# Optimization experiments

Measured on AMD Instinct MI355X. Metric: run time of the kernel, lower is better.

The kernel has to match this reference:

```python
import jax, jax.numpy as jnp
import numpy as np

N_NODES = 50000
N_EDGES = 800000
D = 64               # in_channels
CHEB_ORDER = 16
NUM_GRAPHS = 100
SCALES = [2, 4, 8, 16]           # 2**i for i in 1..4
FENG = np.array([4, 8, 9, 12, 13, 14])  # feng_filters()


def _cheb_coeffs(order):
    # FastScatterW1._get_coeffs with N = cheb_order + 1
    N = order + 1
    a1, a2 = 1.0, 1.0        # a_arange = [0, 2]
    tmp = np.arange(N)
    num = np.cos(np.pi * (tmp + 0.5) / N)
    xs = a1 * num + a2
    c = np.zeros((len(SCALES), N))
    for si, s in enumerate(SCALES):
        ker = np.sqrt(np.clip((1.0 - xs) ** (s // 2) - (1.0 - xs) ** s, 0.0, None))
        for o in range(N):
            c[si, o] = 2.0 / N * np.dot(ker, np.cos(np.pi * o * (tmp + 0.5) / N))
    return c.T.astype(np.float32)  # [order+1, n_scales]


def setup_inputs():
    key = jax.random.key(0)
    k1, k2 = jax.random.split(key)
    x = jax.random.normal(k1, (N_NODES, D), dtype=jnp.float32)
    edge_index = jax.random.randint(k2, (2, N_EDGES), 0, N_NODES, dtype=jnp.int32)
    # 100 contiguous graphs of 500 nodes each (sorted, every graph non-empty)
    batch = (jnp.arange(N_NODES) // (N_NODES // NUM_GRAPHS)).astype(jnp.int32)
    return {"x": x, "edge_index": edge_index, "batch": batch}


def _cheb_apply(x, rows, cols, w, coeffs, n):
    # ChebConvFixed recurrence with arange=[0,1] -> a1 = a2 = 0.5.
    # x: [N, F] -> out: [S, N, F]
    def prop(h):  # scatter-add message passing: out[c] += w_e * h[row_e]
        return jax.ops.segment_sum(w[:, None] * h[rows], cols, num_segments=n)
    Tx0 = x
    Tx1 = 2.0 * prop(x) - x                      # (prop(x) - a2*Tx0)/a1
    out = coeffs[0][:, None, None] * (0.5 * Tx0) + coeffs[1][:, None, None] * Tx1
    def step(carry, c_k):
        t0, t1, acc = carry
        t2 = 4.0 * (prop(t1) - 0.5 * t1) - t0    # 2/a1 * (prop - a2*t1) - t0
        return (t1, t2, acc + c_k[:, None, None] * t2), None
    (_, _, out), _ = jax.lax.scan(step, (Tx0, Tx1, out), coeffs[2:])
    return out


def _scatter_moments(f, batch, g):
    # f: [N, F] node features, vectorized version of scatter_moments(..., 4)
    cnt = jax.ops.segment_sum(jnp.ones((f.shape[0],), f.dtype), batch, num_segments=g)[:, None]
    mean = jax.ops.segment_sum(f, batch, num_segments=g) / cnt
    dev = f - mean[batch]
    m2 = jax.ops.segment_sum(dev ** 2, batch, num_segments=g) / cnt
    m3 = jax.ops.segment_sum(dev ** 3, batch, num_segments=g) / cnt
    m4 = jax.ops.segment_sum(dev ** 4, batch, num_segments=g) / cnt
    safe = jnp.where(m2 > 0, m2, 1.0)
    skew = jnp.where(m2 > 0, m3 / safe ** 1.5, 0.0)
    skew = jnp.where(skew > 1e15, 0.0, skew)
    kurt = jnp.where(m2 > 0, m4 / safe ** 2 - 3.0, -3.0)
    kurt = jnp.where(kurt > 1e15, -3.0, kurt)
    return jnp.concatenate([mean, m2, skew, kurt], axis=1)  # [G, 4F]


def reference(x, edge_index, batch):
    n = x.shape[0]
    row, col = edge_index[0], edge_index[1]
    # symmetric normalization: deg from scatter_add of unit weights on col
    deg = jax.ops.segment_sum(jnp.ones((row.shape[0],), x.dtype), col, num_segments=n)
    dh = jnp.where(deg > 0, deg ** -0.5, 0.0)
    ew = dh[row] * dh[col]
    # Original: add_self_loops(+1), /2, then negate and add_self_loops(+1) again:
    # edge weights -> -ew/2 on real edges; net self-loop weight = -0.5 + 1.0 = 0.5.
    loops = jnp.arange(n, dtype=row.dtype)
    rows_all = jnp.concatenate([row, loops])
    cols_all = jnp.concatenate([col, loops])
    w = jnp.concatenate([-0.5 * ew, 0.5 * jnp.ones((n,), x.dtype)])
    coeffs = jnp.asarray(_cheb_coeffs(CHEB_ORDER))  # [K+1, 4]
    # alpha = 0 -> deg0 = deg1 = deg**0 = 1, so pre/post degree scalings are identity.
    d1 = _cheb_apply(x, rows_all, cols_all, w, coeffs, n)              # [4, N, D]
    s1 = jnp.abs(d1)
    h = s1.transpose(1, 0, 2).reshape(n, 4 * D)                         # [N, 4D]
    d2 = _cheb_apply(h, rows_all, cols_all, w, coeffs, n)               # [4, N, 4D]
    s2 = jnp.abs(d2).transpose(1, 0, 2).reshape(n, 16, D)[:, jnp.asarray(FENG)]  # [N, 6, D]
    feat = jnp.concatenate([x[:, None, :], s1.transpose(1, 0, 2), s2], axis=1)  # [N, 11, D]
    return _scatter_moments(feat.reshape(n, -1), batch, NUM_GRAPHS)    # [G, 44*D]
```

## Files before the change

### kernel.cpp

```cpp
#include <hip/hip_runtime.h>
#include <math.h>

#define NN 50000
#define NE 800000
#define NGRAPH 100
#define NPG 500
#define NB_SCAN 196
#define NCHUNK 5
#define NPC 100
#define CHAIN_ELEMS ((size_t)NN * 64)
#define CH4 ((size_t)NN * 16)
#define GRID_PROP (NN / 4)
#define GRID_P163 (NN / 8)

typedef long long ll;
typedef _Float16 h4_t __attribute__((ext_vector_type(4)));
typedef _Float16 h8_t __attribute__((ext_vector_type(8)));

__device__ __forceinline__ void unpack(ll v, int& r, float& w) {
    r = (int)(v & 0xffffffffLL);
    w = __int_as_float((int)(v >> 32));
}

__device__ __forceinline__ float4 f4fma(float w, float4 v, float4 a) {
    a.x += w * v.x; a.y += w * v.y; a.z += w * v.z; a.w += w * v.w;
    return a;
}

__device__ __forceinline__ float4 h4f4(h4_t h) {
    return make_float4((float)h.x, (float)h.y, (float)h.z, (float)h.w);
}

__device__ __forceinline__ h4_t f4h4(float4 v) {
    h4_t h;
    h.x = (_Float16)v.x; h.y = (_Float16)v.y;
    h.z = (_Float16)v.z; h.w = (_Float16)v.w;
    return h;
}


__global__ void k_deg(const int* __restrict__ col, int* __restrict__ degi) {
    int e = blockIdx.x * blockDim.x + threadIdx.x;
    if (e < NE) atomicAdd(&degi[col[e]], 1);
}

__global__ void k_dh(const int* __restrict__ degi, float* __restrict__ dh) {
    int i = blockIdx.x * blockDim.x + threadIdx.x;
    if (i < NN) {
        int d = degi[i];
        dh[i] = d > 0 ? (float)(1.0 / sqrt((double)d)) : 0.0f;
    }
}

__global__ void k_bsum(const int* __restrict__ cnt, int* __restrict__ bsum) {
    __shared__ int sh[256];
    int i = blockIdx.x * 256 + threadIdx.x;
    sh[threadIdx.x] = (i < NN) ? cnt[i] : 0;
    __syncthreads();
    for (int s = 128; s > 0; s >>= 1) {
        if (threadIdx.x < s) sh[threadIdx.x] += sh[threadIdx.x + s];
        __syncthreads();
    }
    if (threadIdx.x == 0) bsum[blockIdx.x] = sh[0];
}

__global__ void k_bscan(const int* __restrict__ bsum, int* __restrict__ boff) {
    __shared__ int sh[2][256];
    int v = (threadIdx.x < NB_SCAN) ? bsum[threadIdx.x] : 0;
    int cur = 0;
    sh[0][threadIdx.x] = v;
    __syncthreads();
    for (int s = 1; s < 256; s <<= 1) {
        int val = sh[cur][threadIdx.x];
        if ((int)threadIdx.x >= s) val += sh[cur][threadIdx.x - s];
        sh[cur ^ 1][threadIdx.x] = val;
        cur ^= 1;
        __syncthreads();
    }
    if (threadIdx.x < NB_SCAN) boff[threadIdx.x] = sh[cur][threadIdx.x] - v;
}

__global__ void k_scan2(const int* __restrict__ cnt, const int* __restrict__ boff,
                        int* __restrict__ off) {
    __shared__ int sh[2][256];
    int i = blockIdx.x * 256 + threadIdx.x;
    int v = (i < NN) ? cnt[i] : 0;
    int cur = 0;
    sh[0][threadIdx.x] = v;
    __syncthreads();
    for (int s = 1; s < 256; s <<= 1) {
        int val = sh[cur][threadIdx.x];
        if ((int)threadIdx.x >= s) val += sh[cur][threadIdx.x - s];
        sh[cur ^ 1][threadIdx.x] = val;
        cur ^= 1;
        __syncthreads();
    }
    if (i < NN) off[i] = boff[blockIdx.x] + sh[cur][threadIdx.x] - v;
}

__global__ void k_fill(const int* __restrict__ row, const int* __restrict__ col,
                       const float* __restrict__ dh, const int* __restrict__ off,
                       int* __restrict__ cursor, ll* __restrict__ csrp) {
    int e = blockIdx.x * blockDim.x + threadIdx.x;
    if (e >= NE) return;
    int r = row[e], c = col[e];
    int pos = off[c] + atomicAdd(&cursor[c], 1);
    float w = dh[r] * dh[c];
    csrp[pos] = ((ll)__float_as_int(w) << 32) | (unsigned int)r;
}


template <bool INIT>
__global__ __launch_bounds__(256) void k_prop(
    const float* __restrict__ Tcur, const float* __restrict__ Tprev,
    float* __restrict__ Tnext, const int* __restrict__ off,
    const int* __restrict__ degi, const ll* __restrict__ csrp) {
    int node = blockIdx.x * 4 + (threadIdx.x >> 6);
    int lane = threadIdx.x & 63;
    int eg = lane >> 4;
    int cq = lane & 15;
    int s = off[node], e = s + degi[node];
    const float* tb = Tcur + (size_t)cq * 4;
    float4 a0 = make_float4(0.f, 0.f, 0.f, 0.f);
    float4 a1 = make_float4(0.f, 0.f, 0.f, 0.f);
    float4 pv = INIT ? make_float4(0.f, 0.f, 0.f, 0.f)
                     : *(const float4*)&Tprev[(size_t)node * 64 + cq * 4];
    int i = s;
    for (; i + 8 <= e; i += 8) {
        int r0, r1; float w0, w1;
        unpack(csrp[i + eg], r0, w0);
        unpack(csrp[i + 4 + eg], r1, w1);
        float4 v0 = *(const float4*)(tb + (size_t)r0 * 64);
        float4 v1 = *(const float4*)(tb + (size_t)r1 * 64);
        a0 = f4fma(w0, v0, a0);
        a1 = f4fma(w1, v1, a1);
    }
    for (; i < e; i += 4) {
        int idx = i + eg;
        bool act = idx < e;
        int r; float w;
        unpack(csrp[act ? idx : (e - 1)], r, w);
        if (!act) w = 0.f;
        float4 v = *(const float4*)(tb + (size_t)r * 64);
        a0 = f4fma(w, v, a0);
    }
    float4 g = make_float4(a0.x + a1.x, a0.y + a1.y, a0.z + a1.z, a0.w + a1.w);
    g.x += __shfl_xor(g.x, 16); g.y += __shfl_xor(g.y, 16);
    g.z += __shfl_xor(g.z, 16); g.w += __shfl_xor(g.w, 16);
    g.x += __shfl_xor(g.x, 32); g.y += __shfl_xor(g.y, 32);
    g.z += __shfl_xor(g.z, 32); g.w += __shfl_xor(g.w, 32);
    float4 t;
    if (INIT) {
        t = make_float4(-g.x, -g.y, -g.z, -g.w);
    } else {
        t = make_float4(-2.f * g.x - pv.x, -2.f * g.y - pv.y,
                        -2.f * g.z - pv.z, -2.f * g.w - pv.w);
    }
    if (eg == 0) *(float4*)&Tnext[(size_t)node * 64 + cq * 4] = t;
}


template <bool INIT>
__global__ __launch_bounds__(256) void k_prop16x3(
    const _Float16* __restrict__ Tcur, const _Float16* __restrict__ Tprev,
    _Float16* __restrict__ Tnext, const int* __restrict__ off,
    const int* __restrict__ degi, const ll* __restrict__ csrp) {
    int wav = blockIdx.x * 4 + (threadIdx.x >> 6);
    int lane = threadIdx.x & 63;
    int ns = lane >> 5;
    int eg = (lane >> 3) & 3;
    int cq = lane & 7;
    int node = wav * 2 + ns;
    int s = off[node], e = s + degi[node];
    const _Float16* tb0 = Tcur + (size_t)cq * 8;
    const _Float16* tb1 = tb0 + CHAIN_ELEMS;
    const _Float16* tb2 = tb0 + 2 * CHAIN_ELEMS;
    float aA[3][8], aB[3][8];
#pragma unroll
    for (int p = 0; p < 3; ++p)
#pragma unroll
        for (int j = 0; j < 8; ++j) { aA[p][j] = 0.f; aB[p][j] = 0.f; }
    int i = s;
    for (; i + 8 <= e; i += 8) {
        int r0, r1; float w0, w1;
        unpack(csrp[i + eg], r0, w0);
        unpack(csrp[i + 4 + eg], r1, w1);
        size_t o0 = (size_t)r0 * 64, o1 = (size_t)r1 * 64;
        h8_t h00 = *(const h8_t*)(tb0 + o0);
        h8_t h01 = *(const h8_t*)(tb1 + o0);
        h8_t h02 = *(const h8_t*)(tb2 + o0);
        h8_t h10 = *(const h8_t*)(tb0 + o1);
        h8_t h11 = *(const h8_t*)(tb1 + o1);
        h8_t h12 = *(const h8_t*)(tb2 + o1);
#pragma unroll
        for (int j = 0; j < 8; ++j) aA[0][j] += w0 * (float)h00[j];
#pragma unroll
        for (int j = 0; j < 8; ++j) aA[1][j] += w0 * (float)h01[j];
#pragma unroll
        for (int j = 0; j < 8; ++j) aA[2][j] += w0 * (float)h02[j];
#pragma unroll
        for (int j = 0; j < 8; ++j) aB[0][j] += w1 * (float)h10[j];
#pragma unroll
        for (int j = 0; j < 8; ++j) aB[1][j] += w1 * (float)h11[j];
#pragma unroll
        for (int j = 0; j < 8; ++j) aB[2][j] += w1 * (float)h12[j];
    }
    for (; i < e; i += 4) {
        int idx = i + eg;
        bool act = idx < e;
        int r; float w;
        unpack(csrp[act ? idx : (e - 1)], r, w);
        if (!act) w = 0.f;
        size_t o = (size_t)r * 64;
        h8_t h0 = *(const h8_t*)(tb0 + o);
        h8_t h1 = *(const h8_t*)(tb1 + o);
        h8_t h2 = *(const h8_t*)(tb2 + o);
#pragma unroll
        for (int j = 0; j < 8; ++j) aA[0][j] += w * (float)h0[j];
#pragma unroll
        for (int j = 0; j < 8; ++j) aA[1][j] += w * (float)h1[j];
#pragma unroll
        for (int j = 0; j < 8; ++j) aA[2][j] += w * (float)h2[j];
    }
    float g[3][8];
#pragma unroll
    for (int p = 0; p < 3; ++p)
#pragma unroll
        for (int j = 0; j < 8; ++j) g[p][j] = aA[p][j] + aB[p][j];
#pragma unroll
    for (int p = 0; p < 3; ++p)
#pragma unroll
        for (int j = 0; j < 8; ++j) {
            g[p][j] += __shfl_xor(g[p][j], 8);
            g[p][j] += __shfl_xor(g[p][j], 16);
        }
    if ((lane & 24) == 0) {
        size_t ob = (size_t)node * 64 + (size_t)cq * 8;
#pragma unroll
        for (int p = 0; p < 3; ++p) {
            size_t o = ob + (size_t)p * CHAIN_ELEMS;
            h8_t t;
            if (INIT) {
#pragma unroll
                for (int j = 0; j < 8; ++j) t[j] = (_Float16)(-g[p][j]);
            } else {
                h8_t ph = *(const h8_t*)&Tprev[o];
#pragma unroll
                for (int j = 0; j < 8; ++j)
                    t[j] = (_Float16)(-2.f * g[p][j] - (float)ph[j]);
            }
            *(h8_t*)&Tnext[o] = t;
        }
    }
}


struct CombCfg {
    float c0[4];
    float ck[4][8];
    int   plane[4];
};

template <int NS, int NT>
__global__ __launch_bounds__(256) void k_combine(
    const float4* __restrict__ src0, const float4* __restrict__ pool,
    float4* __restrict__ accb, _Float16* __restrict__ h16out,
    CombCfg cfg, int first, int doabs) {
    size_t v = (size_t)blockIdx.x * 256 + threadIdx.x;
    float4 tv[NS];
#pragma unroll
    for (int m = 0; m < NS; ++m) tv[m] = pool[(size_t)m * CH4 + v];
    float4 s0 = first ? src0[v] : make_float4(0.f, 0.f, 0.f, 0.f);
#pragma unroll
    for (int t = 0; t < NT; ++t) {
        size_t o = (size_t)cfg.plane[t] * CH4 + v;
        float4 a;
        if (first) {
            float c = cfg.c0[t];
            a = make_float4(c * s0.x, c * s0.y, c * s0.z, c * s0.w);
        } else {
            a = accb[o];
        }
#pragma unroll
        for (int m = 0; m < NS; ++m) a = f4fma(cfg.ck[t][m], tv[m], a);
        if (doabs) a = make_float4(fabsf(a.x), fabsf(a.y), fabsf(a.z), fabsf(a.w));
        accb[o] = a;
        if (doabs && h16out && cfg.plane[t] < 3) {
            size_t eo = (size_t)cfg.plane[t] * CHAIN_ELEMS + v * 4;
            *(h4_t*)&h16out[eo] = f4h4(a);
        }
    }
}


struct Comb316Cfg {
    float c0[6];
    float ck[6][4];
};

__global__ __launch_bounds__(256) void k_comb316(
    const float4* __restrict__ src0, const h4_t* __restrict__ pool,
    h4_t* __restrict__ accb, Comb316Cfg cfg, int first, int doabs) {
    size_t v = (size_t)blockIdx.x * 256 + threadIdx.x;
    float4 tv[4][3];
#pragma unroll
    for (int m = 0; m < 4; ++m)
#pragma unroll
        for (int sp = 0; sp < 3; ++sp)
            tv[m][sp] = h4f4(pool[((size_t)m * 3 + sp) * CH4 + v]);
    float4 s0[3];
    if (first) {
#pragma unroll
        for (int sp = 0; sp < 3; ++sp) s0[sp] = src0[(size_t)sp * CH4 + v];
    }
    const int SP[6] = {0, 0, 0, 1, 1, 2};
    const int PL[6] = {0, 1, 3, 2, 4, 5};
#pragma unroll
    for (int t = 0; t < 6; ++t) {
        size_t o = (size_t)PL[t] * CH4 + v;
        float4 a;
        if (first) {
            float c = cfg.c0[t];
            float4 s = s0[SP[t]];
            a = make_float4(c * s.x, c * s.y, c * s.z, c * s.w);
        } else {
            a = h4f4(accb[o]);
        }
#pragma unroll
        for (int m = 0; m < 4; ++m) a = f4fma(cfg.ck[t][m], tv[m][SP[t]], a);
        if (doabs) a = make_float4(fabsf(a.x), fabsf(a.y), fabsf(a.z), fabsf(a.w));
        accb[o] = f4h4(a);
    }
}


__global__ void k_mompart(const float* __restrict__ x, const float* __restrict__ hacc,
                          const _Float16* __restrict__ acc2, double* __restrict__ pmom) {
    int g = blockIdx.y;
    int c = blockIdx.z;
    int col = blockIdx.x * 256 + threadIdx.x;
    if (col >= 704) return;
    int base = g * NPG + c * NPC;
    double s1 = 0, s2 = 0, s3 = 0, s4 = 0;
    if (col < 320) {
        const float* src;
        int c0;
        if (col < 64) { src = x; c0 = col; }
        else { int p = (col - 64) >> 6; src = hacc + (size_t)p * CHAIN_ELEMS; c0 = (col - 64) & 63; }
        for (int i = 0; i < NPC; ++i) {
            double v = (double)src[(size_t)(base + i) * 64 + c0];
            double v2 = v * v;
            s1 += v; s2 += v2; s3 += v2 * v; s4 += v2 * v2;
        }
    } else {
        int p = (col - 320) >> 6;
        int c0 = (col - 320) & 63;
        const _Float16* src = acc2 + (size_t)p * CHAIN_ELEMS;
        for (int i = 0; i < NPC; ++i) {
            double v = (double)(float)src[(size_t)(base + i) * 64 + c0];
            double v2 = v * v;
            s1 += v; s2 += v2; s3 += v2 * v; s4 += v2 * v2;
        }
    }
    size_t ob = (((size_t)c * NGRAPH + g) * 704 + col) * 4;
    pmom[ob + 0] = s1;
    pmom[ob + 1] = s2;
    pmom[ob + 2] = s3;
    pmom[ob + 3] = s4;
}

__global__ void k_momfin(const double* __restrict__ pmom, float* __restrict__ out) {
    int g = blockIdx.y;
    int col = blockIdx.x * 256 + threadIdx.x;
    if (col >= 704) return;
    double s1 = 0, s2 = 0, s3 = 0, s4 = 0;
    for (int c = 0; c < NCHUNK; ++c) {
        size_t ob = (((size_t)c * NGRAPH + g) * 704 + col) * 4;
        s1 += pmom[ob + 0];
        s2 += pmom[ob + 1];
        s3 += pmom[ob + 2];
        s4 += pmom[ob + 3];
    }
    double n = (double)NPG;
    double mu = s1 / n;
    double E2 = s2 / n, E3 = s3 / n, E4 = s4 / n;
    double m2 = E2 - mu * mu;
    double m3 = E3 - 3.0 * mu * E2 + 2.0 * mu * mu * mu;
    double m4 = E4 - 4.0 * mu * E3 + 6.0 * mu * mu * E2 - 3.0 * mu * mu * mu * mu;
    float m2f = (float)m2;
    float skew = 0.f, kurt = -3.f;
    if (m2f > 0.f) {
        skew = (float)(m3 / (m2 * sqrt(m2)));
        if (skew > 1e15f) skew = 0.f;
        kurt = (float)(m4 / (m2 * m2) - 3.0);
        if (kurt > 1e15f) kurt = -3.f;
    }
    size_t ob = (size_t)g * 2816 + col;
    out[ob]        = (float)mu;
    out[ob + 704]  = m2f;
    out[ob + 1408] = skew;
    out[ob + 2112] = kurt;
}


extern "C" void kernel_launch(void* const* d_in, const int* in_sizes, int n_in,
                              void* d_out, int out_size, void* d_ws, size_t ws_size,
                              hipStream_t stream) {
    const float* x = (const float*)d_in[0];
    const int* ei  = (const int*)d_in[1];
    const int* row = ei;
    const int* col = ei + NE;
    float* out = (float*)d_out;

    float C[17][4];
    {
        const int Nc = 17;
        const int scales[4] = {2, 4, 8, 16};
        for (int si = 0; si < 4; ++si) {
            double ker[17];
            for (int j = 0; j < Nc; ++j) {
                double num = cos(M_PI * (j + 0.5) / Nc);
                double b = -num;
                double v = pow(b, (double)(scales[si] / 2)) - pow(b, (double)scales[si]);
                if (v < 0) v = 0;
                ker[j] = sqrt(v);
            }
            for (int o = 0; o < Nc; ++o) {
                double acc = 0;
                for (int j = 0; j < Nc; ++j) acc += ker[j] * cos(M_PI * o * (j + 0.5) / Nc);
                C[o][si] = (float)(2.0 / Nc * acc);
            }
        }
    }

    int*   degi; float* dh; int* off; int* cursor; int* bsum; int* boff;
    ll*    csrp; char* ub = nullptr;
    float* hacc; _Float16* acc2;
    int CAD1 = 8;
    const size_t H16B  = ((size_t)3 * CHAIN_ELEMS * 2 + 255) & ~(size_t)255;
    const size_t P16B  = ((size_t)12 * CHAIN_ELEMS * 2 + 255) & ~(size_t)255;
    const size_t PMOMB = (size_t)NCHUNK * NGRAPH * 704 * 4 * 8;
    size_t H16OFF = 0;
    for (int attempt = 0; attempt < 2; ++attempt) {
        CAD1 = (attempt == 0) ? 8 : 4;
        size_t POOLB = ((size_t)CAD1 * CHAIN_ELEMS * 4 + 255) & ~(size_t)255;
        H16OFF = (POOLB > P16B) ? POOLB : P16B;
        size_t UNB = H16OFF + H16B;
        if (PMOMB > UNB) UNB = PMOMB;
        char* p = (char*)d_ws;
        auto alloc = [&](size_t bytes) -> void* {
            void* r = (void*)p;
            p += (bytes + 255) & ~(size_t)255;
            return r;
        };
        degi   = (int*)alloc((size_t)NN * 4);
        dh     = (float*)alloc((size_t)NN * 4);
        off    = (int*)alloc((size_t)NN * 4);
        cursor = (int*)alloc((size_t)NN * 4);
        bsum   = (int*)alloc((size_t)NB_SCAN * 4);
        boff   = (int*)alloc((size_t)NB_SCAN * 4);
        csrp   = (ll*)alloc((size_t)NE * 8);
        ub     = (char*)alloc(UNB);
        hacc   = (float*)alloc((size_t)4 * CHAIN_ELEMS * 4);
        acc2   = (_Float16*)alloc((size_t)6 * CHAIN_ELEMS * 2);
        if ((size_t)(p - (char*)d_ws) <= ws_size) break;
    }
    float*    pool   = (float*)ub;
    _Float16* pool16 = (_Float16*)ub;
    _Float16* h16    = (_Float16*)(ub + H16OFF);
    double*   pmom   = (double*)ub;

    hipMemsetAsync(degi, 0, (size_t)NN * 4, stream);
    hipMemsetAsync(cursor, 0, (size_t)NN * 4, stream);

    k_deg  <<<(NE + 255) / 256, 256, 0, stream>>>(col, degi);
    k_dh   <<<(NN + 255) / 256, 256, 0, stream>>>(degi, dh);
    k_bsum <<<NB_SCAN, 256, 0, stream>>>(degi, bsum);
    k_bscan<<<1, 256, 0, stream>>>(bsum, boff);
    k_scan2<<<NB_SCAN, 256, 0, stream>>>(degi, boff, off);
    k_fill <<<(NE + 255) / 256, 256, 0, stream>>>(row, col, dh, off, cursor, csrp);

    const int GRID_C = (int)(CH4 / 256);

    auto slot = [&](int k) {
        return pool + (size_t)((k - 1) & (CAD1 - 1)) * CHAIN_ELEMS;
    };

    {
        const int scl[4] = {0, 1, 2, 3};
        k_prop<true><<<GRID_PROP, 256, 0, stream>>>(x, nullptr, slot(1),
                                                    off, degi, csrp);
        for (int k = 2; k <= 16; ++k) {
            const float* Tprev = (k == 2) ? x : slot(k - 2);
            k_prop<false><<<GRID_PROP, 256, 0, stream>>>(slot(k - 1), Tprev,
                                                         slot(k), off, degi, csrp);
            if ((k % CAD1) == 0) {
                CombCfg cfg;
                for (int t = 0; t < 4; ++t) {
                    int si = scl[t];
                    cfg.c0[t] = 0.5f * C[0][si];
                    cfg.plane[t] = t;
                    for (int m = 0; m < CAD1; ++m)
                        cfg.ck[t][m] = C[k - CAD1 + 1 + m][si];
                }
                int first = (k == CAD1) ? 1 : 0;
                int doabs = (k == 16) ? 1 : 0;
                _Float16* ho = doabs ? h16 : nullptr;
                if (CAD1 == 8)
                    k_combine<8, 4><<<GRID_C, 256, 0, stream>>>(
                        (const float4*)x, (const float4*)pool, (float4*)hacc,
                        ho, cfg, first, doabs);
                else
                    k_combine<4, 4><<<GRID_C, 256, 0, stream>>>(
                        (const float4*)x, (const float4*)pool, (float4*)hacc,
                        ho, cfg, first, doabs);
            }
        }
    }

    {
        auto slot3 = [&](int k) {
            return pool16 + (size_t)((k - 1) & 3) * 3 * CHAIN_ELEMS;
        };
        k_prop16x3<true><<<GRID_P163, 256, 0, stream>>>(h16, nullptr, slot3(1),
                                                        off, degi, csrp);
        for (int k = 2; k <= 16; ++k) {
            const _Float16* Tprev = (k == 2) ? h16 : slot3(k - 2);
            k_prop16x3<false><<<GRID_P163, 256, 0, stream>>>(slot3(k - 1), Tprev,
                                                             slot3(k), off, degi, csrp);
            if ((k % 4) == 0) {
                Comb316Cfg cfg;
                const int SI[6] = {1, 2, 3, 2, 3, 3};
                for (int t = 0; t < 6; ++t) {
                    cfg.c0[t] = 0.5f * C[0][SI[t]];
                    for (int m = 0; m < 4; ++m) cfg.ck[t][m] = C[k - 3 + m][SI[t]];
                }
                k_comb316<<<GRID_C, 256, 0, stream>>>(
                    (const float4*)hacc, (const h4_t*)pool16, (h4_t*)acc2,
                    cfg, (k == 4) ? 1 : 0, (k == 16) ? 1 : 0);
            }
        }
    }

    dim3 mg1(3, NGRAPH, NCHUNK);
    k_mompart<<<mg1, 256, 0, stream>>>(x, hacc, acc2, pmom);
    dim3 mg2(3, NGRAPH);
    k_momfin<<<mg2, 256, 0, stream>>>(pmom, out);
}
```

Measured before the change: 1.567 ms.

## Store first-stage Chebyshev chain in fp16 and remap prop to two nodes per wave

The first-layer Chebyshev recurrence now keeps x and every T_k in half precision, with fp32 accumulation. The propagation kernel is rewritten so each wave handles two nodes with 8-wide half vectors, and the combine kernel reads the fp16 pool. This halves the bytes per gathered neighbour row in the bandwidth-bound sparse propagation and shrinks the pool buffer, which removes the CAD1 fallback. The cost is fp16 rounding error compounding across the 16-step recurrence, plus an extra conversion pass over x.

Result: faster. 1.385 ms (-11.6%).

```diff
diff --git a/kernel.cpp b/kernel.cpp
--- a/kernel.cpp
+++ b/kernel.cpp
@@ -10,7 +10,6 @@
 #define NPC 100
 #define CHAIN_ELEMS ((size_t)NN * 64)
 #define CH4 ((size_t)NN * 16)
-#define GRID_PROP (NN / 4)
 #define GRID_P163 (NN / 8)
 
 typedef long long ll;
@@ -109,31 +108,40 @@
     csrp[pos] = ((ll)__float_as_int(w) << 32) | (unsigned int)r;
 }
 
+__global__ void k_tohalf(const float* __restrict__ src, _Float16* __restrict__ dst) {
+    size_t i = ((size_t)blockIdx.x * 256 + threadIdx.x) * 4;
+    float4 v = *(const float4*)&src[i];
+    *(h4_t*)&dst[i] = f4h4(v);
+}
+
 
 template <bool INIT>
-__global__ __launch_bounds__(256) void k_prop(
-    const float* __restrict__ Tcur, const float* __restrict__ Tprev,
-    float* __restrict__ Tnext, const int* __restrict__ off,
+__global__ __launch_bounds__(256) void k_prop16s(
+    const _Float16* __restrict__ Tcur, const _Float16* __restrict__ Tprev,
+    _Float16* __restrict__ Tnext, const int* __restrict__ off,
     const int* __restrict__ degi, const ll* __restrict__ csrp) {
-    int node = blockIdx.x * 4 + (threadIdx.x >> 6);
+    int wav = blockIdx.x * 4 + (threadIdx.x >> 6);
     int lane = threadIdx.x & 63;
-    int eg = lane >> 4;
-    int cq = lane & 15;
+    int ns = lane >> 5;
+    int eg = (lane >> 3) & 3;
+    int cq = lane & 7;
+    int node = wav * 2 + ns;
     int s = off[node], e = s + degi[node];
-    const float* tb = Tcur + (size_t)cq * 4;
-    float4 a0 = make_float4(0.f, 0.f, 0.f, 0.f);
-    float4 a1 = make_float4(0.f, 0.f, 0.f, 0.f);
-    float4 pv = INIT ? make_float4(0.f, 0.f, 0.f, 0.f)
-                     : *(const float4*)&Tprev[(size_t)node * 64 + cq * 4];
+    const _Float16* tb = Tcur + (size_t)cq * 8;
+    float accA[8], accB[8];
+#pragma unroll
+    for (int j = 0; j < 8; ++j) { accA[j] = 0.f; accB[j] = 0.f; }
     int i = s;
     for (; i + 8 <= e; i += 8) {
         int r0, r1; float w0, w1;
         unpack(csrp[i + eg], r0, w0);
         unpack(csrp[i + 4 + eg], r1, w1);
-        float4 v0 = *(const float4*)(tb + (size_t)r0 * 64);
-        float4 v1 = *(const float4*)(tb + (size_t)r1 * 64);
-        a0 = f4fma(w0, v0, a0);
-        a1 = f4fma(w1, v1, a1);
+        h8_t h0 = *(const h8_t*)(tb + (size_t)r0 * 64);
+        h8_t h1 = *(const h8_t*)(tb + (size_t)r1 * 64);
+#pragma unroll
+        for (int j = 0; j < 8; ++j) accA[j] += w0 * (float)h0[j];
+#pragma unroll
+        for (int j = 0; j < 8; ++j) accB[j] += w1 * (float)h1[j];
     }
     for (; i < e; i += 4) {
         int idx = i + eg;
@@ -141,22 +149,32 @@
         int r; float w;
         unpack(csrp[act ? idx : (e - 1)], r, w);
         if (!act) w = 0.f;
-        float4 v = *(const float4*)(tb + (size_t)r * 64);
-        a0 = f4fma(w, v, a0);
-    }
-    float4 g = make_float4(a0.x + a1.x, a0.y + a1.y, a0.z + a1.z, a0.w + a1.w);
-    g.x += __shfl_xor(g.x, 16); g.y += __shfl_xor(g.y, 16);
-    g.z += __shfl_xor(g.z, 16); g.w += __shfl_xor(g.w, 16);
-    g.x += __shfl_xor(g.x, 32); g.y += __shfl_xor(g.y, 32);
-    g.z += __shfl_xor(g.z, 32); g.w += __shfl_xor(g.w, 32);
-    float4 t;
-    if (INIT) {
-        t = make_float4(-g.x, -g.y, -g.z, -g.w);
-    } else {
-        t = make_float4(-2.f * g.x - pv.x, -2.f * g.y - pv.y,
-                        -2.f * g.z - pv.z, -2.f * g.w - pv.w);
-    }
-    if (eg == 0) *(float4*)&Tnext[(size_t)node * 64 + cq * 4] = t;
+        h8_t h = *(const h8_t*)(tb + (size_t)r * 64);
+#pragma unroll
+        for (int j = 0; j < 8; ++j) accA[j] += w * (float)h[j];
+    }
+    float g[8];
+#pragma unroll
+    for (int j = 0; j < 8; ++j) g[j] = accA[j] + accB[j];
+#pragma unroll
+    for (int j = 0; j < 8; ++j) {
+        g[j] += __shfl_xor(g[j], 8);
+        g[j] += __shfl_xor(g[j], 16);
+    }
+    if ((lane & 24) == 0) {
+        size_t o = (size_t)node * 64 + (size_t)cq * 8;
+        h8_t t;
+        if (INIT) {
+#pragma unroll
+            for (int j = 0; j < 8; ++j) t[j] = (_Float16)(-g[j]);
+        } else {
+            h8_t ph = *(const h8_t*)&Tprev[o];
+#pragma unroll
+            for (int j = 0; j < 8; ++j)
+                t[j] = (_Float16)(-2.f * g[j] - (float)ph[j]);
+        }
+        *(h8_t*)&Tnext[o] = t;
+    }
 }
 
 
@@ -262,14 +280,14 @@
 };
 
 template <int NS, int NT>
-__global__ __launch_bounds__(256) void k_combine(
-    const float4* __restrict__ src0, const float4* __restrict__ pool,
+__global__ __launch_bounds__(256) void k_combine16p1(
+    const float4* __restrict__ src0, const h4_t* __restrict__ pool,
     float4* __restrict__ accb, _Float16* __restrict__ h16out,
     CombCfg cfg, int first, int doabs) {
     size_t v = (size_t)blockIdx.x * 256 + threadIdx.x;
     float4 tv[NS];
 #pragma unroll
-    for (int m = 0; m < NS; ++m) tv[m] = pool[(size_t)m * CH4 + v];
+    for (int m = 0; m < NS; ++m) tv[m] = h4f4(pool[(size_t)m * CH4 + v]);
     float4 s0 = first ? src0[v] : make_float4(0.f, 0.f, 0.f, 0.f);
 #pragma unroll
     for (int t = 0; t < NT; ++t) {
@@ -435,16 +453,13 @@
 
     int*   degi; float* dh; int* off; int* cursor; int* bsum; int* boff;
     ll*    csrp; char* ub = nullptr;
-    float* hacc; _Float16* acc2;
-    int CAD1 = 8;
+    _Float16* x16; float* hacc; _Float16* acc2;
     const size_t H16B  = ((size_t)3 * CHAIN_ELEMS * 2 + 255) & ~(size_t)255;
+    const size_t P1B   = ((size_t)8 * CHAIN_ELEMS * 2 + 255) & ~(size_t)255;
     const size_t P16B  = ((size_t)12 * CHAIN_ELEMS * 2 + 255) & ~(size_t)255;
     const size_t PMOMB = (size_t)NCHUNK * NGRAPH * 704 * 4 * 8;
-    size_t H16OFF = 0;
-    for (int attempt = 0; attempt < 2; ++attempt) {
-        CAD1 = (attempt == 0) ? 8 : 4;
-        size_t POOLB = ((size_t)CAD1 * CHAIN_ELEMS * 4 + 255) & ~(size_t)255;
-        H16OFF = (POOLB > P16B) ? POOLB : P16B;
+    size_t H16OFF = (P1B > P16B) ? P1B : P16B;
+    {
         size_t UNB = H16OFF + H16B;
         if (PMOMB > UNB) UNB = PMOMB;
         char* p = (char*)d_ws;
@@ -461,11 +476,11 @@
         boff   = (int*)alloc((size_t)NB_SCAN * 4);
         csrp   = (ll*)alloc((size_t)NE * 8);
         ub     = (char*)alloc(UNB);
+        x16    = (_Float16*)alloc(CHAIN_ELEMS * 2);
         hacc   = (float*)alloc((size_t)4 * CHAIN_ELEMS * 4);
         acc2   = (_Float16*)alloc((size_t)6 * CHAIN_ELEMS * 2);
-        if ((size_t)(p - (char*)d_ws) <= ws_size) break;
-    }
-    float*    pool   = (float*)ub;
+    }
+    _Float16* pool1  = (_Float16*)ub;
     _Float16* pool16 = (_Float16*)ub;
     _Float16* h16    = (_Float16*)(ub + H16OFF);
     double*   pmom   = (double*)ub;
@@ -481,39 +496,34 @@
     k_fill <<<(NE + 255) / 256, 256, 0, stream>>>(row, col, dh, off, cursor, csrp);
 
     const int GRID_C = (int)(CH4 / 256);
-
-    auto slot = [&](int k) {
-        return pool + (size_t)((k - 1) & (CAD1 - 1)) * CHAIN_ELEMS;
-    };
+    k_tohalf<<<GRID_C, 256, 0, stream>>>(x, x16);
 
     {
+        auto slot1 = [&](int k) {
+            return pool1 + (size_t)((k - 1) & 7) * CHAIN_ELEMS;
+        };
         const int scl[4] = {0, 1, 2, 3};
-        k_prop<true><<<GRID_PROP, 256, 0, stream>>>(x, nullptr, slot(1),
-                                                    off, degi, csrp);
+        k_prop16s<true><<<GRID_P163, 256, 0, stream>>>(x16, nullptr, slot1(1),
+                                                       off, degi, csrp);
         for (int k = 2; k <= 16; ++k) {
-            const float* Tprev = (k == 2) ? x : slot(k - 2);
-            k_prop<false><<<GRID_PROP, 256, 0, stream>>>(slot(k - 1), Tprev,
-                                                         slot(k), off, degi, csrp);
-            if ((k % CAD1) == 0) {
+            const _Float16* Tprev = (k == 2) ? x16 : slot1(k - 2);
+            k_prop16s<false><<<GRID_P163, 256, 0, stream>>>(slot1(k - 1), Tprev,
+                                                            slot1(k), off, degi, csrp);
+            if ((k % 8) == 0) {
                 CombCfg cfg;
                 for (int t = 0; t < 4; ++t) {
                     int si = scl[t];
                     cfg.c0[t] = 0.5f * C[0][si];
                     cfg.plane[t] = t;
-                    for (int m = 0; m < CAD1; ++m)
-                        cfg.ck[t][m] = C[k - CAD1 + 1 + m][si];
+                    for (int m = 0; m < 8; ++m)
+                        cfg.ck[t][m] = C[k - 7 + m][si];
                 }
-                int first = (k == CAD1) ? 1 : 0;
+                int first = (k == 8) ? 1 : 0;
                 int doabs = (k == 16) ? 1 : 0;
                 _Float16* ho = doabs ? h16 : nullptr;
-                if (CAD1 == 8)
-                    k_combine<8, 4><<<GRID_C, 256, 0, stream>>>(
-                        (const float4*)x, (const float4*)pool, (float4*)hacc,
-                        ho, cfg, first, doabs);
-                else
-                    k_combine<4, 4><<<GRID_C, 256, 0, stream>>>(
-                        (const float4*)x, (const float4*)pool, (float4*)hacc,
-                        ho, cfg, first, doabs);
+                k_combine16p1<8, 4><<<GRID_C, 256, 0, stream>>>(
+                    (const float4*)x, (const h4_t*)pool1, (float4*)hacc,
+                    ho, cfg, first, doabs);
             }
         }
     }
```
